# Optimization experiments

Measured on AMD Instinct MI355X. Metric: run time of the kernel, lower is better.

Reference implementation:

```python
import jax, jax.numpy as jnp
import numpy as np

B, C, H, W = 8, 320, 64, 64      # query feature map
S_KV, D_KV = 77, 1024            # key/value (text) tokens
HEADS, DIM_HEAD = 8, 64
INNER = HEADS * DIM_HEAD         # 512


def setup_inputs() -> dict:
    key = jax.random.key(0)
    ks = jax.random.split(key, 7)
    return {
        "query": jax.random.normal(ks[0], (B, C, H, W), dtype=jnp.float32),
        "key_value": jax.random.normal(ks[1], (B, S_KV, D_KV), dtype=jnp.float32),
        "Wq": jax.random.normal(ks[2], (C, INNER), dtype=jnp.float32) * (C ** -0.5),
        "Wk": jax.random.normal(ks[3], (D_KV, INNER), dtype=jnp.float32) * (D_KV ** -0.5),
        "Wv": jax.random.normal(ks[4], (D_KV, INNER), dtype=jnp.float32) * (D_KV ** -0.5),
        "Wo": jax.random.normal(ks[5], (INNER, C), dtype=jnp.float32) * (INNER ** -0.5),
        "bo": jnp.zeros((C,), dtype=jnp.float32),
    }


def reference(query, key_value, Wq, Wk, Wv, Wo, bo):
    b, c, h, w = query.shape
    n = h * w
    # [B,C,H,W] -> [B,N,C]
    q_flat = query.reshape(b, c, n).transpose(0, 2, 1)
    # projections, then split heads: [B, S, heads, dim_head]
    q = (q_flat @ Wq).reshape(b, n, HEADS, DIM_HEAD)
    k = (key_value @ Wk).reshape(b, S_KV, HEADS, DIM_HEAD)
    v = (key_value @ Wv).reshape(b, S_KV, HEADS, DIM_HEAD)
    scale = DIM_HEAD ** -0.5
    # attn logits: [B, heads, N, S_kv]
    logits = jnp.einsum('bnhd,bshd->bhns', q, k) * scale
    attn = jax.nn.softmax(logits, axis=-1)
    # weighted values -> merge heads: [B, N, inner]
    out = jnp.einsum('bhns,bshd->bnhd', attn, v).reshape(b, n, INNER)
    out = out @ Wo + bo  # dropout p=0.0 is identity
    # [B,N,C] -> [B,C,H,W]
    return out.transpose(0, 2, 1).reshape(b, c, h, w)
```

## Files before the change

### kernel.cpp

```cpp
#include <hip/hip_runtime.h>
#include <hip/hip_bf16.h>
#include <stdint.h>

#define BB     8
#define CC     320
#define NN     4096
#define SKV    77
#define HEADS  8
#define INNER  512
#define SCALE  0.125f

typedef float f32x4  __attribute__((ext_vector_type(4)));
typedef short bf16x8 __attribute__((ext_vector_type(8)));
typedef short s16x4  __attribute__((ext_vector_type(4)));

static __device__ __forceinline__ short f2bf(float f) {
  unsigned u = __float_as_uint(f);
  return (short)((u + 0x7fffu + ((u >> 16) & 1u)) >> 16);
}

static __device__ __forceinline__ void gll16(void* lds, const void* g) {
  auto gp = reinterpret_cast<const uint32_t __attribute__((address_space(1)))*>(
      reinterpret_cast<uintptr_t>(g));
  auto lp = reinterpret_cast<uint32_t __attribute__((address_space(3)))*>(
      reinterpret_cast<uintptr_t>(lds));
  __builtin_amdgcn_global_load_lds(gp, lp, 16, 0, 0);
}

__global__ __launch_bounds__(256) void prep_kernel(
    const float* __restrict__ kv, const float* __restrict__ Wk,
    const float* __restrict__ Wv, const float* __restrict__ Wq,
    const float* __restrict__ Wo, const float* __restrict__ query,
    short* __restrict__ kv_bf, short* __restrict__ Wk_t,
    short* __restrict__ Wv_t, short* __restrict__ Wq_t,
    short* __restrict__ Wo_t, short* __restrict__ X_bf,
    unsigned* __restrict__ zero_base) {
  __shared__ float T[64 * 65];
  const int blk = blockIdx.x, t = threadIdx.x;
  if (blk < 616) {
    const int base = blk * 1024;
    #pragma unroll
    for (int i = 0; i < 4; ++i) kv_bf[base + i*256 + t] = f2bf(kv[base + i*256 + t]);
    return;
  }
  if (blk >= 1392) {
    const int blk2 = blk - 1392;
    const int b = blk2 / 320, r = blk2 % 320;
    const int nt = r / 5, ct = r % 5;
    const int tl = t & 63, rb = t >> 6;
    #pragma unroll
    for (int i = 0; i < 16; ++i) {
      const int c = rb + i*4;
      T[c*65 + tl] = query[((size_t)(b*CC + ct*64 + c))*NN + nt*64 + tl];
    }
    __syncthreads();
    #pragma unroll
    for (int i = 0; i < 16; ++i) {
      const int n = rb + i*4;
      X_bf[((size_t)(b*NN + nt*64 + n))*CC + ct*64 + tl] = f2bf(T[tl*65 + n]);
    }
    return;
  }
  if (blk >= 952) {
    const int base = (blk - 952) * 1024;
    #pragma unroll
    for (int i = 0; i < 4; ++i) zero_base[base + i*256 + t] = 0u;
    return;
  }
  const float* src; short* dst; int RS, CS, kt, ct; float scl = 1.0f;
  if (blk < 872) {
    const int tile = blk - 616;
    const bool isK = tile < 128;
    const int tt = isK ? tile : tile - 128;
    src = isK ? Wk : Wv; dst = isK ? Wk_t : Wv_t;
    RS = 1024; CS = 512; kt = tt >> 3; ct = tt & 7;
  } else if (blk < 912) {
    const int tt = blk - 872;
    src = Wq; dst = Wq_t; RS = 320; CS = 512; kt = tt >> 3; ct = tt & 7;
    scl = SCALE;
  } else {
    const int tt = blk - 912;
    src = Wo; dst = Wo_t; RS = 512; CS = 320; kt = tt / 5; ct = tt % 5;
  }
  const int cl = t & 63, rb = t >> 6;
  #pragma unroll
  for (int i = 0; i < 16; ++i)
    T[(rb + i*4)*65 + cl] = src[(size_t)(kt*64 + rb + i*4)*CS + ct*64 + cl];
  __syncthreads();
  #pragma unroll
  for (int i = 0; i < 16; ++i) {
    const int nl = rb + i*4;
    dst[(size_t)(ct*64 + nl)*RS + kt*64 + cl] = f2bf(T[cl*65 + nl] * scl);
  }
}

__global__ __launch_bounds__(256) void kvproj_kernel(
    const short* __restrict__ kv_bf, const short* __restrict__ Wk_t,
    const short* __restrict__ Wv_t, short* __restrict__ K_ws,
    short* __restrict__ V_ws) {
  const int t = threadIdx.x, w = t >> 6, lane = t & 63;
  const int l15 = lane & 15, q = lane >> 4;
  const int m0 = (blockIdx.x * 4 + w) * 16;
  const int y = blockIdx.y;
  const bool isK = (y < 8);
  const int h = y & 7;
  const short* __restrict__ Wt = isK ? Wk_t : Wv_t;
  const int arow = (m0 + l15 < 616) ? (m0 + l15) : 615;

  const f32x4 z = {0.f, 0.f, 0.f, 0.f};
  f32x4 acc[4] = {z, z, z, z};
  for (int k0 = 0; k0 < 1024; k0 += 32) {
    const bf16x8 a = *(const bf16x8*)(kv_bf + arow*1024 + k0 + q*8);
    #pragma unroll
    for (int nt = 0; nt < 4; ++nt) {
      const int n = h*64 + nt*16 + l15;
      const bf16x8 bfr = *(const bf16x8*)(Wt + n*1024 + k0 + q*8);
      acc[nt] = __builtin_amdgcn_mfma_f32_16x16x32_bf16(a, bfr, acc[nt], 0, 0, 0);
    }
  }
  #pragma unroll
  for (int nt = 0; nt < 4; ++nt) {
    const int d = nt*16 + l15;
    #pragma unroll
    for (int r = 0; r < 4; ++r) {
      const int row = m0 + q*4 + r;
      if (row < 616) {
        const int b = (int)(((unsigned)row * 54472u) >> 22);
        const int s = row - b*77;
        if (isK) K_ws[((b*8 + h)*80 + s)*64 + d] = f2bf(acc[nt][r]);
        else     V_ws[((b*8 + h)*64 + d)*96 + s] = f2bf(acc[nt][r]);
      }
    }
  }
}

__global__ __launch_bounds__(256, 2) void qproj_kernel(
    const short* __restrict__ X_bf, const short* __restrict__ Wq_t,
    short* __restrict__ Q_ws) {
  const int t = threadIdx.x, w = t >> 6, lane = t & 63;
  const int l15 = lane & 15, q = lane >> 4;
  const int m0 = (blockIdx.x >> 1) * 128;
  const int n0 = (blockIdx.x & 1) * 256;
  const int wm = w & 1, wn = w >> 1;

  __shared__ short tile[12288];

  const f32x4 z = {0.f, 0.f, 0.f, 0.f};
  f32x4 acc[8][4];
  #pragma unroll
  for (int jt = 0; jt < 8; ++jt)
    #pragma unroll
    for (int tt = 0; tt < 4; ++tt) acc[jt][tt] = z;

  for (int it = 0; it < 10; ++it) {
    const int k0 = it * 32;
    if (it) __syncthreads();
    #pragma unroll
    for (int p = 0; p < 2; ++p) {
      const int f = p*256 + t, row = f >> 2, c4 = f & 3;
      gll16(tile + f*8, X_bf + (size_t)(m0 + row)*320 + k0 + c4*8);
    }
    #pragma unroll
    for (int p = 0; p < 4; ++p) {
      const int f = p*256 + t, row = f >> 2, c4 = f & 3;
      gll16(tile + 4096 + f*8, Wq_t + (size_t)(n0 + row)*320 + k0 + c4*8);
    }
    __syncthreads();
    bf16x8 a[8], bb[4];
    #pragma unroll
    for (int jt = 0; jt < 8; ++jt)
      a[jt] = *(const bf16x8*)(tile + 4096 + (wn*128 + jt*16 + l15)*32 + q*8);
    #pragma unroll
    for (int tt = 0; tt < 4; ++tt)
      bb[tt] = *(const bf16x8*)(tile + (wm*64 + tt*16 + l15)*32 + q*8);
    #pragma unroll
    for (int jt = 0; jt < 8; ++jt)
      #pragma unroll
      for (int tt = 0; tt < 4; ++tt)
        acc[jt][tt] = __builtin_amdgcn_mfma_f32_16x16x32_bf16(a[jt], bb[tt], acc[jt][tt], 0, 0, 0);
  }
  #pragma unroll
  for (int tt = 0; tt < 4; ++tt) {
    short* rowp = Q_ws + (size_t)(m0 + wm*64 + tt*16 + l15)*512 + n0 + wn*128;
    #pragma unroll
    for (int jt = 0; jt < 8; ++jt) {
      s16x4 pv;
      #pragma unroll
      for (int r = 0; r < 4; ++r) pv[r] = f2bf(acc[jt][tt][r]);
      *(s16x4*)(rowp + jt*16 + q*4) = pv;
    }
  }
}

__global__ __launch_bounds__(256) void attncore_kernel(
    const short* __restrict__ Q_ws, const short* __restrict__ K_ws,
    const short* __restrict__ V_ws, short* __restrict__ O_ws) {
  const int t = threadIdx.x, w = t >> 6, lane = t & 63;
  const int unit = blockIdx.x * 4 + w;
  const int h = unit & 7;
  const int g = unit >> 3;
  const int b = g >> 7;
  const int n0 = (g & 127) * 32;
  const int l15 = lane & 15, q = lane >> 4;

  __shared__ short scr[4 * 32 * 104];
  short* scrw = scr + w * 32 * 104;
  for (int i = lane; i < 32*104/2; i += 64) ((unsigned*)scrw)[i] = 0u;

  const short* __restrict__ Kh = K_ws + (size_t)(b*8 + h) * 80 * 64;
  const short* __restrict__ Vh = V_ws + (size_t)(b*8 + h) * 64 * 96;
  size_t tokrow[2];
  #pragma unroll
  for (int nt = 0; nt < 2; ++nt) tokrow[nt] = (size_t)(b*NN + n0 + nt*16 + l15);

  const f32x4 z = {0.f, 0.f, 0.f, 0.f};
  f32x4 qk[2][5];
  #pragma unroll
  for (int nt = 0; nt < 2; ++nt)
    #pragma unroll
    for (int st = 0; st < 5; ++st) qk[nt][st] = z;
  #pragma unroll
  for (int f = 0; f < 2; ++f) {
    bf16x8 bq[2];
    #pragma unroll
    for (int nt = 0; nt < 2; ++nt)
      bq[nt] = *(const bf16x8*)(Q_ws + tokrow[nt]*512 + h*64 + f*32 + q*8);
    #pragma unroll
    for (int st = 0; st < 5; ++st) {
      const bf16x8 a = *(const bf16x8*)(Kh + (st*16 + l15)*64 + f*32 + q*8);
      #pragma unroll
      for (int nt = 0; nt < 2; ++nt)
        qk[nt][st] = __builtin_amdgcn_mfma_f32_16x16x32_bf16(a, bq[nt], qk[nt][st], 0, 0, 0);
    }
  }

  #pragma unroll
  for (int nt = 0; nt < 2; ++nt) {
    float mx = -1e30f;
    #pragma unroll
    for (int st = 0; st < 5; ++st)
      #pragma unroll
      for (int r = 0; r < 4; ++r) {
        const int s = st*16 + q*4 + r;
        const float vv = (s < SKV) ? qk[nt][st][r] : -1e30f;
        qk[nt][st][r] = vv;
        mx = fmaxf(mx, vv);
      }
    mx = fmaxf(mx, __shfl_xor(mx, 16));
    mx = fmaxf(mx, __shfl_xor(mx, 32));
    float sum = 0.f;
    #pragma unroll
    for (int st = 0; st < 5; ++st)
      #pragma unroll
      for (int r = 0; r < 4; ++r) {
        const int s = st*16 + q*4 + r;
        const float e = (s < SKV) ? __expf(qk[nt][st][r] - mx) : 0.f;
        qk[nt][st][r] = e;
        sum += e;
      }
    sum += __shfl_xor(sum, 16);
    sum += __shfl_xor(sum, 32);
    const float inv = 1.0f / sum;
    #pragma unroll
    for (int st = 0; st < 5; ++st) {
      s16x4 pv;
      #pragma unroll
      for (int r = 0; r < 4; ++r) pv[r] = f2bf(qk[nt][st][r] * inv);
      *(s16x4*)(scrw + (nt*16 + l15)*104 + st*16 + q*4) = pv;
    }
  }

  f32x4 ov[2][4];
  #pragma unroll
  for (int nt = 0; nt < 2; ++nt)
    #pragma unroll
    for (int dt = 0; dt < 4; ++dt) ov[nt][dt] = z;
  #pragma unroll
  for (int f = 0; f < 3; ++f) {
    bf16x8 bp[2];
    #pragma unroll
    for (int nt = 0; nt < 2; ++nt)
      bp[nt] = *(const bf16x8*)(scrw + (nt*16 + l15)*104 + f*32 + q*8);
    #pragma unroll
    for (int dt = 0; dt < 4; ++dt) {
      const bf16x8 a = *(const bf16x8*)(Vh + (dt*16 + l15)*96 + f*32 + q*8);
      #pragma unroll
      for (int nt = 0; nt < 2; ++nt)
        ov[nt][dt] = __builtin_amdgcn_mfma_f32_16x16x32_bf16(a, bp[nt], ov[nt][dt], 0, 0, 0);
    }
  }
  #pragma unroll
  for (int nt = 0; nt < 2; ++nt)
    #pragma unroll
    for (int dt = 0; dt < 4; ++dt) {
      s16x4 pv;
      #pragma unroll
      for (int r = 0; r < 4; ++r) pv[r] = f2bf(ov[nt][dt][r]);
      *(s16x4*)(O_ws + tokrow[nt]*512 + h*64 + dt*16 + q*4) = pv;
    }
}

__global__ __launch_bounds__(256) void outproj_kernel(
    const short* __restrict__ O_ws, const short* __restrict__ Wo_t,
    const float* __restrict__ bo, float* __restrict__ out) {
  const int t = threadIdx.x, w = t >> 6, lane = t & 63;
  const int l15 = lane & 15, q = lane >> 4;
  const int t0 = blockIdx.x * 64;

  __shared__ short tile[12288];

  const f32x4 z = {0.f, 0.f, 0.f, 0.f};
  f32x4 acc[5][4];
  #pragma unroll
  for (int mt = 0; mt < 5; ++mt)
    #pragma unroll
    for (int nt = 0; nt < 4; ++nt) acc[mt][nt] = z;

  for (int it = 0; it < 16; ++it) {
    const int k0 = it * 32;
    if (it) __syncthreads();
    #pragma unroll
    for (int p = 0; p < 5; ++p) {
      const int f = p*256 + t, row = f >> 2, c4 = f & 3;
      gll16(tile + f*8, Wo_t + (size_t)row*512 + k0 + c4*8);
    }
    {
      const int row = t >> 2, c4 = t & 3;
      gll16(tile + 10240 + t*8, O_ws + (size_t)(t0 + row)*512 + k0 + c4*8);
    }
    __syncthreads();
    bf16x8 a[5], bb[4];
    #pragma unroll
    for (int mt = 0; mt < 5; ++mt)
      a[mt] = *(const bf16x8*)(tile + (w*80 + mt*16 + l15)*32 + q*8);
    #pragma unroll
    for (int nt = 0; nt < 4; ++nt)
      bb[nt] = *(const bf16x8*)(tile + 10240 + (nt*16 + l15)*32 + q*8);
    #pragma unroll
    for (int mt = 0; mt < 5; ++mt)
      #pragma unroll
      for (int nt = 0; nt < 4; ++nt)
        acc[mt][nt] = __builtin_amdgcn_mfma_f32_16x16x32_bf16(a[mt], bb[nt], acc[mt][nt], 0, 0, 0);
  }
  const int b = t0 >> 12, n = t0 & 4095;
  #pragma unroll
  for (int mt = 0; mt < 5; ++mt)
    #pragma unroll
    for (int r = 0; r < 4; ++r) {
      const int c = w*80 + mt*16 + q*4 + r;
      const float bv = bo[c];
      float* rowp = out + ((size_t)(b*CC + c))*NN + n;
      #pragma unroll
      for (int nt = 0; nt < 4; ++nt)
        rowp[nt*16 + l15] = acc[mt][nt][r] + bv;
    }
}

extern "C" void kernel_launch(void* const* d_in, const int* in_sizes, int n_in,
                              void* d_out, int out_size, void* d_ws, size_t ws_size,
                              hipStream_t stream) {
  const float* query = (const float*)d_in[0];
  const float* kv    = (const float*)d_in[1];
  const float* Wq    = (const float*)d_in[2];
  const float* Wk    = (const float*)d_in[3];
  const float* Wv    = (const float*)d_in[4];
  const float* Wo    = (const float*)d_in[5];
  const float* bo    = (const float*)d_in[6];
  float* out = (float*)d_out;

  char* p = (char*)d_ws;
  short* K_ws  = (short*)(p);
  short* V_ws  = (short*)(p +   819200);
  short* Wq_t  = (short*)(p +  1802240);
  short* Wo_t  = (short*)(p +  2129920);
  short* Q_ws  = (short*)(p +  2457600);
  char* pb = p + 36012032;
  short* X_bf  = (short*)(pb);
  short* kv_bf = (short*)(pb + 20971520);
  short* Wk_t  = (short*)(pb + 22233088);
  short* Wv_t  = (short*)(pb + 23281664);
  short* O_ws  = (short*)(pb);

  prep_kernel<<<3952, 256, 0, stream>>>(kv, Wk, Wv, Wq, Wo, query, kv_bf,
                                        Wk_t, Wv_t, Wq_t, Wo_t, X_bf,
                                        (unsigned*)p);
  kvproj_kernel<<<dim3(10, 16), 256, 0, stream>>>(kv_bf, Wk_t, Wv_t, K_ws, V_ws);
  qproj_kernel<<<512, 256, 0, stream>>>(X_bf, Wq_t, Q_ws);
  attncore_kernel<<<2048, 256, 0, stream>>>(Q_ws, K_ws, V_ws, O_ws);
  outproj_kernel<<<512, 256, 0, stream>>>(O_ws, Wo_t, bo, out);
}
```

Baseline: 195.4 us.

## Fuse query transpose into Q projection and merge KV projection into same launch

Removes the separate query NCHW→NHWC bf16 transpose pass from the prep kernel. The Q projection now reads fp32 query directly, converting and transposing it into a padded LDS tile. The K/V projection blocks are folded into the same launch as extra blocks, each wave handling four head/type combos, which drops one kernel launch. This avoids writing and re-reading the X_bf intermediate, at the cost of strided fp32 global reads and a 512-thread block that loads the full Wq tile each K step.

```diff
diff --git a/kernel.cpp b/kernel.cpp
--- a/kernel.cpp
+++ b/kernel.cpp
@@ -9,6 +9,7 @@
 #define HEADS  8
 #define INNER  512
 #define SCALE  0.125f
+#define XSTR   40
 
 typedef float f32x4  __attribute__((ext_vector_type(4)));
 typedef short bf16x8 __attribute__((ext_vector_type(8)));
@@ -30,10 +31,9 @@
 __global__ __launch_bounds__(256) void prep_kernel(
     const float* __restrict__ kv, const float* __restrict__ Wk,
     const float* __restrict__ Wv, const float* __restrict__ Wq,
-    const float* __restrict__ Wo, const float* __restrict__ query,
-    short* __restrict__ kv_bf, short* __restrict__ Wk_t,
-    short* __restrict__ Wv_t, short* __restrict__ Wq_t,
-    short* __restrict__ Wo_t, short* __restrict__ X_bf,
+    const float* __restrict__ Wo, short* __restrict__ kv_bf,
+    short* __restrict__ Wk_t, short* __restrict__ Wv_t,
+    short* __restrict__ Wq_t, short* __restrict__ Wo_t,
     unsigned* __restrict__ zero_base) {
   __shared__ float T[64 * 65];
   const int blk = blockIdx.x, t = threadIdx.x;
@@ -41,24 +41,6 @@
     const int base = blk * 1024;
     #pragma unroll
     for (int i = 0; i < 4; ++i) kv_bf[base + i*256 + t] = f2bf(kv[base + i*256 + t]);
-    return;
-  }
-  if (blk >= 1392) {
-    const int blk2 = blk - 1392;
-    const int b = blk2 / 320, r = blk2 % 320;
-    const int nt = r / 5, ct = r % 5;
-    const int tl = t & 63, rb = t >> 6;
-    #pragma unroll
-    for (int i = 0; i < 16; ++i) {
-      const int c = rb + i*4;
-      T[c*65 + tl] = query[((size_t)(b*CC + ct*64 + c))*NN + nt*64 + tl];
-    }
-    __syncthreads();
-    #pragma unroll
-    for (int i = 0; i < 16; ++i) {
-      const int n = rb + i*4;
-      X_bf[((size_t)(b*NN + nt*64 + n))*CC + ct*64 + tl] = f2bf(T[tl*65 + n]);
-    }
     return;
   }
   if (blk >= 952) {
@@ -94,96 +76,102 @@
   }
 }
 
-__global__ __launch_bounds__(256) void kvproj_kernel(
+__global__ __launch_bounds__(512) void qproj_kernel(
+    const float* __restrict__ query, const short* __restrict__ Wq_t,
     const short* __restrict__ kv_bf, const short* __restrict__ Wk_t,
-    const short* __restrict__ Wv_t, short* __restrict__ K_ws,
-    short* __restrict__ V_ws) {
+    const short* __restrict__ Wv_t, short* __restrict__ Q_ws,
+    short* __restrict__ K_ws, short* __restrict__ V_ws) {
   const int t = threadIdx.x, w = t >> 6, lane = t & 63;
   const int l15 = lane & 15, q = lane >> 4;
-  const int m0 = (blockIdx.x * 4 + w) * 16;
-  const int y = blockIdx.y;
-  const bool isK = (y < 8);
-  const int h = y & 7;
-  const short* __restrict__ Wt = isK ? Wk_t : Wv_t;
-  const int arow = (m0 + l15 < 616) ? (m0 + l15) : 615;
-
   const f32x4 z = {0.f, 0.f, 0.f, 0.f};
-  f32x4 acc[4] = {z, z, z, z};
-  for (int k0 = 0; k0 < 1024; k0 += 32) {
-    const bf16x8 a = *(const bf16x8*)(kv_bf + arow*1024 + k0 + q*8);
-    #pragma unroll
-    for (int nt = 0; nt < 4; ++nt) {
-      const int n = h*64 + nt*16 + l15;
-      const bf16x8 bfr = *(const bf16x8*)(Wt + n*1024 + k0 + q*8);
-      acc[nt] = __builtin_amdgcn_mfma_f32_16x16x32_bf16(a, bfr, acc[nt], 0, 0, 0);
-    }
-  }
-  #pragma unroll
-  for (int nt = 0; nt < 4; ++nt) {
-    const int d = nt*16 + l15;
-    #pragma unroll
-    for (int r = 0; r < 4; ++r) {
-      const int row = m0 + q*4 + r;
-      if (row < 616) {
-        const int b = (int)(((unsigned)row * 54472u) >> 22);
-        const int s = row - b*77;
-        if (isK) K_ws[((b*8 + h)*80 + s)*64 + d] = f2bf(acc[nt][r]);
-        else     V_ws[((b*8 + h)*64 + d)*96 + s] = f2bf(acc[nt][r]);
+
+  if (blockIdx.x >= 256) {
+    const int g = (blockIdx.x - 256) * 8 + w;
+    const int mt = g % 40, yg = g / 40;
+    const int m0 = mt * 16;
+    const int arow = (m0 + l15 < 616) ? (m0 + l15) : 615;
+    for (int i = 0; i < 4; ++i) {
+      const int y = yg * 4 + i;
+      const bool isK = (y < 8);
+      const int h = y & 7;
+      const short* __restrict__ Wt = isK ? Wk_t : Wv_t;
+      f32x4 acc[4] = {z, z, z, z};
+      for (int k0 = 0; k0 < 1024; k0 += 32) {
+        const bf16x8 a = *(const bf16x8*)(kv_bf + arow*1024 + k0 + q*8);
+        #pragma unroll
+        for (int nt = 0; nt < 4; ++nt) {
+          const int n = h*64 + nt*16 + l15;
+          const bf16x8 bfr = *(const bf16x8*)(Wt + n*1024 + k0 + q*8);
+          acc[nt] = __builtin_amdgcn_mfma_f32_16x16x32_bf16(a, bfr, acc[nt], 0, 0, 0);
+        }
       }
-    }
-  }
-}
-
-__global__ __launch_bounds__(256, 2) void qproj_kernel(
-    const short* __restrict__ X_bf, const short* __restrict__ Wq_t,
-    short* __restrict__ Q_ws) {
-  const int t = threadIdx.x, w = t >> 6, lane = t & 63;
-  const int l15 = lane & 15, q = lane >> 4;
-  const int m0 = (blockIdx.x >> 1) * 128;
-  const int n0 = (blockIdx.x & 1) * 256;
-  const int wm = w & 1, wn = w >> 1;
-
-  __shared__ short tile[12288];
-
-  const f32x4 z = {0.f, 0.f, 0.f, 0.f};
-  f32x4 acc[8][4];
-  #pragma unroll
-  for (int jt = 0; jt < 8; ++jt)
-    #pragma unroll
-    for (int tt = 0; tt < 4; ++tt) acc[jt][tt] = z;
+      #pragma unroll
+      for (int nt = 0; nt < 4; ++nt) {
+        const int d = nt*16 + l15;
+        #pragma unroll
+        for (int r = 0; r < 4; ++r) {
+          const int row = m0 + q*4 + r;
+          if (row < 616) {
+            const int b = (int)(((unsigned)row * 54472u) >> 22);
+            const int s = row - b*77;
+            if (isK) K_ws[((b*8 + h)*80 + s)*64 + d] = f2bf(acc[nt][r]);
+            else     V_ws[((b*8 + h)*64 + d)*96 + s] = f2bf(acc[nt][r]);
+          }
+        }
+      }
+    }
+    return;
+  }
+
+  const int gtok = blockIdx.x * 128;
+  const int b = gtok >> 12, n0 = gtok & 4095;
+  __shared__ short smem[128*XSTR + 512*32];
+  short* Xt = smem;
+  short* Wt = smem + 128*XSTR;
+
+  f32x4 acc[4][8];
+  #pragma unroll
+  for (int jt = 0; jt < 4; ++jt)
+    #pragma unroll
+    for (int tt = 0; tt < 8; ++tt) acc[jt][tt] = z;
 
   for (int it = 0; it < 10; ++it) {
     const int k0 = it * 32;
     if (it) __syncthreads();
     #pragma unroll
-    for (int p = 0; p < 2; ++p) {
-      const int f = p*256 + t, row = f >> 2, c4 = f & 3;
-      gll16(tile + f*8, X_bf + (size_t)(m0 + row)*320 + k0 + c4*8);
-    }
-    #pragma unroll
     for (int p = 0; p < 4; ++p) {
-      const int f = p*256 + t, row = f >> 2, c4 = f & 3;
-      gll16(tile + 4096 + f*8, Wq_t + (size_t)(n0 + row)*320 + k0 + c4*8);
+      const int f = p*512 + t, row = f >> 2, c4 = f & 3;
+      gll16(Wt + f*8, Wq_t + (size_t)row*320 + k0 + c4*8);
+    }
+    #pragma unroll
+    for (int i = 0; i < 2; ++i) {
+      const int idx = i*512 + t;
+      const int tok = idx & 127, cq = idx >> 7;
+      const float* qp = query + ((size_t)(b*CC + k0 + cq*4))*NN + n0 + tok;
+      s16x4 pv;
+      #pragma unroll
+      for (int j = 0; j < 4; ++j) pv[j] = f2bf(qp[(size_t)j*NN]);
+      *(s16x4*)(Xt + tok*XSTR + cq*4) = pv;
     }
     __syncthreads();
-    bf16x8 a[8], bb[4];
-    #pragma unroll
-    for (int jt = 0; jt < 8; ++jt)
-      a[jt] = *(const bf16x8*)(tile + 4096 + (wn*128 + jt*16 + l15)*32 + q*8);
-    #pragma unroll
-    for (int tt = 0; tt < 4; ++tt)
-      bb[tt] = *(const bf16x8*)(tile + (wm*64 + tt*16 + l15)*32 + q*8);
-    #pragma unroll
-    for (int jt = 0; jt < 8; ++jt)
-      #pragma unroll
-      for (int tt = 0; tt < 4; ++tt)
+    bf16x8 a[4], bb[8];
+    #pragma unroll
+    for (int jt = 0; jt < 4; ++jt)
+      a[jt] = *(const bf16x8*)(Wt + (w*64 + jt*16 + l15)*32 + q*8);
+    #pragma unroll
+    for (int tt = 0; tt < 8; ++tt)
+      bb[tt] = *(const bf16x8*)(Xt + (tt*16 + l15)*XSTR + q*8);
+    #pragma unroll
+    for (int jt = 0; jt < 4; ++jt)
+      #pragma unroll
+      for (int tt = 0; tt < 8; ++tt)
         acc[jt][tt] = __builtin_amdgcn_mfma_f32_16x16x32_bf16(a[jt], bb[tt], acc[jt][tt], 0, 0, 0);
   }
   #pragma unroll
-  for (int tt = 0; tt < 4; ++tt) {
-    short* rowp = Q_ws + (size_t)(m0 + wm*64 + tt*16 + l15)*512 + n0 + wn*128;
-    #pragma unroll
-    for (int jt = 0; jt < 8; ++jt) {
+  for (int tt = 0; tt < 8; ++tt) {
+    short* rowp = Q_ws + (size_t)(gtok + tt*16 + l15)*512 + w*64;
+    #pragma unroll
+    for (int jt = 0; jt < 4; ++jt) {
       s16x4 pv;
       #pragma unroll
       for (int r = 0; r < 4; ++r) pv[r] = f2bf(acc[jt][tt][r]);
@@ -375,17 +363,15 @@
   short* Wo_t  = (short*)(p +  2129920);
   short* Q_ws  = (short*)(p +  2457600);
   char* pb = p + 36012032;
-  short* X_bf  = (short*)(pb);
-  short* kv_bf = (short*)(pb + 20971520);
-  short* Wk_t  = (short*)(pb + 22233088);
-  short* Wv_t  = (short*)(pb + 23281664);
   short* O_ws  = (short*)(pb);
-
-  prep_kernel<<<3952, 256, 0, stream>>>(kv, Wk, Wv, Wq, Wo, query, kv_bf,
-                                        Wk_t, Wv_t, Wq_t, Wo_t, X_bf,
-                                        (unsigned*)p);
-  kvproj_kernel<<<dim3(10, 16), 256, 0, stream>>>(kv_bf, Wk_t, Wv_t, K_ws, V_ws);
-  qproj_kernel<<<512, 256, 0, stream>>>(X_bf, Wq_t, Q_ws);
+  short* kv_bf = (short*)(pb + 33554432);
+  short* Wk_t  = (short*)(pb + 34816000);
+  short* Wv_t  = (short*)(pb + 35864576);
+
+  prep_kernel<<<1392, 256, 0, stream>>>(kv, Wk, Wv, Wq, Wo, kv_bf, Wk_t, Wv_t,
+                                        Wq_t, Wo_t, (unsigned*)p);
+  qproj_kernel<<<276, 512, 0, stream>>>(query, Wq_t, kv_bf, Wk_t, Wv_t,
+                                        Q_ws, K_ws, V_ws);
   attncore_kernel<<<2048, 256, 0, stream>>>(Q_ws, K_ws, V_ws, O_ws);
   outproj_kernel<<<512, 256, 0, stream>>>(O_ws, Wo_t, bo, out);
 }
```

Measured after the change: 314.3 us. 60.9% more time.
